# Optimization experiments

Measured on AMD Instinct MI355X. Metric: run time of the kernel, lower is better.

## Reference

```python
import jax, jax.numpy as jnp
import numpy as np

N_GT = 20000          # num_genotypes
N_T = 50              # num timepoints
N_POS = 2000          # num_positions
ALPHA = 4             # len_alphabet
TIME_STEP = 5         # spacing between consecutive timepoints (generations)
ZERO_THR = 1e-6       # hparams['zero threshold']
DILUTION = 0.3        # hparams['dilution threshold']


def setup_inputs() -> dict:
    key = jax.random.key(0)
    k1, k2, k3 = jax.random.split(key, 3)
    fitness = jnp.ones((N_GT,), jnp.float32) * -1.0 + jax.random.normal(k1, (N_GT,), jnp.float32) * 0.01
    fq_mat = jax.random.normal(k2, (N_T, N_GT), jnp.float32)
    genotypes_tensor = jax.random.bernoulli(k3, 0.5, (N_GT, N_POS * ALPHA)).astype(jnp.float32)
    return {"fitness": fitness, "fq_mat": fq_mat, "genotypes_tensor": genotypes_tensor}


def _safe_log(x, m):
    # log(x) where mask m is true, 0 elsewhere (grad-safe)
    return jnp.where(m, jnp.log(jnp.where(m, x, 1.0)), 0.0)


def reference(fitness, fq_mat, genotypes_tensor):
    fqm = jax.nn.softmax(fq_mat, axis=1)                       # (n_t, n_gt)

    # Marginals: (n_t, n_pos*alpha)
    pred_marginals = (fqm @ genotypes_tensor) / N_POS + 1e-10
    log_pred_marginals = jnp.log(pred_marginals)

    # --- Fitness loss: replicator dynamics between consecutive timepoints ---
    p0s = fqm[:-1]                                             # (n_t-1, n_gt)
    p1s = fqm[1:]                                              # (n_t-1, n_gt)
    mask = p0s >= ZERO_THR                                     # dynamic masking -> weights
    fmask = mask.astype(fqm.dtype)
    p0m = p0s * fmask
    p1m = p1s * fmask
    weight = p1m.sum(axis=1)                                   # (n_t-1,)
    np1 = p1m / weight[:, None]                                # normalized target dist

    present_fitness = jnp.exp(fitness)[None, :] * fmask        # (n_t-1, n_gt)

    # time_step replicator sub-steps (uniform spacing -> fixed unrolled loop)
    input_ps = p0m
    for _ in range(TIME_STEP):
        mean_pop_fitness = jnp.sum(input_ps * present_fitness, axis=1, keepdims=True)
        input_ps = input_ps * (present_fitness / mean_pop_fitness)

    pos = np1 > 0
    kl = jnp.sum(jnp.where(pos, np1 * (_safe_log(np1, pos) - _safe_log(input_ps, pos)), 0.0), axis=1)
    loss_t = weight * kl
    # skip timepoints with weight < dilution threshold
    fitness_loss = jnp.sum(jnp.where(weight >= DILUTION, loss_t, 0.0)) / (N_T - 1)
    fitness_loss = fitness_loss.reshape(1)

    # --- Sparsity (negative skew) loss ---
    m = fqm.mean(axis=1, keepdims=True)
    unnorm_skew = ((fqm - m) ** 3).mean(axis=1)                # (n_t,)
    fq_sparsity_loss = (-unnorm_skew.sum() / N_T).reshape(1)

    return log_pred_marginals, fitness_loss, fq_sparsity_loss
```

## Files before the change

kernel.cpp:

```cpp
#include <hip/hip_runtime.h>
#include <cfloat>
#include <cstdint>

#define N_GT 20000
#define N_T 50
#define NPA 8000
#define N_POS 2000
#define KSTEPS 625
#define KTILE 32
#define PBLK 256
#define FB 512
#define NE 40
#define SCH 2500

typedef __attribute__((ext_vector_type(8))) short short8;
typedef __attribute__((ext_vector_type(4))) float f32x4;

__device__ __forceinline__ float wave_sum(float v) {
#pragma unroll
    for (int o = 32; o > 0; o >>= 1) v += __shfl_down(v, o, 64);
    return v;
}
__device__ float block_sum(float v, float* red) {
    int lane = threadIdx.x & 63, wid = threadIdx.x >> 6, nw = blockDim.x >> 6;
    v = wave_sum(v);
    __syncthreads();
    if (lane == 0) red[wid] = v;
    __syncthreads();
    if (wid == 0) {
        float x = (lane < nw) ? red[lane] : 0.f;
        x = wave_sum(x);
        if (lane == 0) red[0] = x;
    }
    __syncthreads();
    return red[0];
}

__global__ __launch_bounds__(256) void softmax_sum_kernel(
    const float* __restrict__ fq, float* __restrict__ rowsum) {
    __shared__ float red[8];
    int row = blockIdx.x >> 3, c = blockIdx.x & 7;
    const float* p = fq + (size_t)row * N_GT + c * SCH;
    float s = 0.f;
    for (int i = threadIdx.x; i < SCH; i += 256) s += __expf(p[i]);
    s = block_sum(s, red);
    if (threadIdx.x == 0) rowsum[blockIdx.x] = s;
}

__global__ __launch_bounds__(256) void softmax_write_kernel(
    const float* __restrict__ fq, const float* __restrict__ rowsum,
    float* __restrict__ fqm, unsigned short* __restrict__ fqmb,
    float* __restrict__ out) {
    __shared__ float red[8];
    int row = blockIdx.x >> 3, c = blockIdx.x & 7;
    float S = 0.f;
#pragma unroll
    for (int j = 0; j < 8; ++j) S += rowsum[row * 8 + j];
    float inv = 1.f / S;

    const float* p = fq + (size_t)row * N_GT + c * SCH;
    float* ym = fqm + (size_t)row * N_GT + c * SCH;
    unsigned short* yb = fqmb + (size_t)row * N_GT + c * SCH;
    const float mean = 1.f / (float)N_GT;
    float skew = 0.f;
    for (int i = threadIdx.x; i < SCH; i += 256) {
        float y = __expf(p[i]) * inv;
        ym[i] = y;
        unsigned ub = __float_as_uint(y);
        yb[i] = (unsigned short)((ub + 0x7FFFu + ((ub >> 16) & 1u)) >> 16);
        float d = y - mean;
        skew += d * d * d;
    }
    skew = block_sum(skew, red);
    if (threadIdx.x == 0)
        atomicAdd(out + 400001, skew * (-1.f / ((float)N_GT * (float)N_T)));
}

__global__ __launch_bounds__(FB) void fitness_kernel(
    const float* __restrict__ fqm, const float* __restrict__ fitness,
    float* __restrict__ out) {
    __shared__ float red[8];
    int t = blockIdx.x;
    const float* p0 = fqm + (size_t)t * N_GT;
    const float* p1 = p0 + N_GT;

    float p0m[NE], p1m[NE], l5f[NE];
    float wsum = 0.f, s5 = 0.f;
#pragma unroll
    for (int j = 0; j < NE; ++j) {
        int g = threadIdx.x + j * FB;
        bool in = g < N_GT;
        float a = in ? p0[g] : 0.f;
        float b = in ? p1[g] : 0.f;
        bool m = in && (a >= 1e-6f);
        p0m[j] = m ? a : 0.f;
        p1m[j] = m ? b : 0.f;
        l5f[j] = in ? 5.f * fitness[g] : 0.f;
        wsum += p1m[j];
        s5 += p0m[j] * __expf(l5f[j]);
    }
    float weight = block_sum(wsum, red);
    float S5 = block_sum(s5, red);
    float lS5 = __logf(S5);
    float invw = 1.f / weight;

    float kls = 0.f;
#pragma unroll
    for (int j = 0; j < NE; ++j) {
        if (p1m[j] > 0.f) {
            float np1 = p1m[j] * invw;
            float lips = __logf(p0m[j]) + l5f[j] - lS5;
            kls += np1 * (__logf(np1) - lips);
        }
    }
    float kl = block_sum(kls, red);
    if (threadIdx.x == 0 && weight >= 0.3f)
        atomicAdd(out + 400000, weight * kl * (1.f / (float)(N_T - 1)));
}

__global__ __launch_bounds__(256, 2) void gemm_mfma_kernel(
    const float* __restrict__ B, const unsigned short* __restrict__ Abf,
    float* __restrict__ partial, int ch) {
    __shared__ __align__(16) float lds[2][KTILE][PBLK];
    const int tid = threadIdx.x;
    const int l = tid & 63, w = tid >> 6;
    const int ln = l & 15, kq = l >> 4;
    const int kq8 = kq * 8;
    const int woff = w * 64;
    const int pblk = blockIdx.x * PBLK;
    const int s = blockIdx.y;

    const int ks0 = s * ch;
    int ks1 = ks0 + ch; if (ks1 > KSTEPS) ks1 = KSTEPS;
    const int nk = ks1 - ks0;
    if (nk <= 0) return;

    int scol = pblk + l * 4;
    if (scol > NPA - 4) scol = NPA - 4;

    const unsigned short* abase = Abf + (size_t)ln * N_GT;

    f32x4 acc[4][4];
#pragma unroll
    for (int mt = 0; mt < 4; ++mt)
#pragma unroll
        for (int nt = 0; nt < 4; ++nt)
            acc[mt][nt] = (f32x4){0.f, 0.f, 0.f, 0.f};

    short8 a0[4], a1[4];

#define STAGE(BUF, KS) do {                                                    \
    const float* gsrc_ = B + (size_t)(KS) * (KTILE * NPA) + scol;              \
    _Pragma("unroll") for (int it_ = 0; it_ < 8; ++it_) {                      \
        int row_ = w * 8 + it_;                                                \
        __builtin_amdgcn_global_load_lds(                                      \
            (const __attribute__((address_space(1))) void*)(gsrc_ + (size_t)row_ * NPA), \
            (__attribute__((address_space(3))) void*)&lds[BUF][row_][0],       \
            16, 0, 0);                                                         \
    }                                                                          \
} while (0)

#define LOADA(AV, KS) do {                                                     \
    const int k0_ = (KS) * 32 + kq8;                                           \
    _Pragma("unroll") for (int mt_ = 0; mt_ < 4; ++mt_)                        \
        AV[mt_] = *(const short8*)(abase + (size_t)(mt_ * 16) * N_GT + k0_);   \
} while (0)

#define COMPUTE(BUF, AV) do {                                                  \
    f32x4 f_[8];                                                               \
    _Pragma("unroll") for (int j_ = 0; j_ < 8; ++j_)                           \
        f_[j_] = *(const f32x4*)&lds[BUF][kq8 + j_][woff + ln * 4];            \
    _Pragma("unroll") for (int nt_ = 0; nt_ < 4; ++nt_) {                      \
        short8 bb_;                                                            \
        _Pragma("unroll") for (int j_ = 0; j_ < 8; ++j_)                       \
            bb_[j_] = (short)(__float_as_uint(f_[j_][nt_]) >> 16);             \
        _Pragma("unroll") for (int mt_ = 0; mt_ < 4; ++mt_)                    \
            acc[mt_][nt_] = __builtin_amdgcn_mfma_f32_16x16x32_bf16(           \
                AV[mt_], bb_, acc[mt_][nt_], 0, 0, 0);                         \
    }                                                                          \
} while (0)

    STAGE(0, ks0);
    LOADA(a0, ks0);
    int i = 0;
    for (; i + 1 < nk; i += 2) {
        __syncthreads();
        STAGE(1, ks0 + i + 1);
        LOADA(a1, ks0 + i + 1);
        COMPUTE(0, a0);
        __syncthreads();
        if (i + 2 < nk) { STAGE(0, ks0 + i + 2); LOADA(a0, ks0 + i + 2); }
        COMPUTE(1, a1);
    }
    if (i < nk) {
        __syncthreads();
        COMPUTE(0, a0);
    }

#undef STAGE
#undef LOADA
#undef COMPUTE

    const int rbase = kq * 4;
    const int pst = pblk + woff + ln * 4;
    float* ps = partial + (size_t)s * (N_T * NPA);
    if (pst < NPA) {
#pragma unroll
        for (int mt = 0; mt < 4; ++mt) {
#pragma unroll
            for (int r = 0; r < 4; ++r) {
                int t = mt * 16 + rbase + r;
                if (t < N_T) {
                    float4 v = {acc[mt][0][r], acc[mt][1][r],
                                acc[mt][2][r], acc[mt][3][r]};
                    *reinterpret_cast<float4*>(ps + (size_t)t * NPA + pst) = v;
                }
            }
        }
    }
}

__global__ __launch_bounds__(256) void reduce_log_kernel(
    const float4* __restrict__ partial, float4* __restrict__ out, int ns) {
    int i = blockIdx.x * 256 + threadIdx.x;
    if (i >= (N_T * NPA) / 4) return;
    float4 s = {0.f, 0.f, 0.f, 0.f};
    for (int k = 0; k < ns; ++k) {
        float4 v = partial[(size_t)k * ((N_T * NPA) / 4) + i];
        s.x += v.x; s.y += v.y; s.z += v.z; s.w += v.w;
    }
    const float r = 1.f / (float)N_POS;
    float4 o;
    o.x = __logf(s.x * r + 1e-10f);
    o.y = __logf(s.y * r + 1e-10f);
    o.z = __logf(s.z * r + 1e-10f);
    o.w = __logf(s.w * r + 1e-10f);
    out[i] = o;
}

extern "C" void kernel_launch(void* const* d_in, const int* in_sizes, int n_in,
                              void* d_out, int out_size, void* d_ws, size_t ws_size,
                              hipStream_t stream) {
    const float* fitness = (const float*)d_in[0];
    const float* fq_mat  = (const float*)d_in[1];
    const float* geno    = (const float*)d_in[2];
    float* out = (float*)d_out;

    char* ws = (char*)d_ws;
    float* fqm           = (float*)ws;
    unsigned short* fqmb = (unsigned short*)(ws + 4000000);
    float* rowsum        = (float*)(ws + 6560000);
    float* partial       = (float*)(ws + 6561600);

    int ns = 16;
    while (ns > 1 && (size_t)6561600 + (size_t)ns * 1600000 > ws_size) ns >>= 1;
    int ch = (KSTEPS + ns - 1) / ns;

    hipMemsetAsync((char*)d_out + (size_t)400000 * sizeof(float), 0, 2 * sizeof(float), stream);
    hipMemsetAsync((char*)fqmb + (size_t)N_T * N_GT * sizeof(unsigned short), 0,
                   (size_t)14 * N_GT * sizeof(unsigned short), stream);

    hipLaunchKernelGGL(softmax_sum_kernel, dim3(N_T * 8), dim3(256), 0, stream,
                       fq_mat, rowsum);
    hipLaunchKernelGGL(softmax_write_kernel, dim3(N_T * 8), dim3(256), 0, stream,
                       fq_mat, rowsum, fqm, fqmb, out);
    hipLaunchKernelGGL(fitness_kernel, dim3(N_T - 1), dim3(FB), 0, stream,
                       fqm, fitness, out);
    hipLaunchKernelGGL(gemm_mfma_kernel, dim3(NPA / PBLK + 1, ns), dim3(256), 0, stream,
                       geno, fqmb, partial, ch);
    hipLaunchKernelGGL(reduce_log_kernel, dim3(((N_T * NPA) / 4 + 255) / 256), dim3(256), 0, stream,
                       (const float4*)partial, (float4*)out, ns);
}
```

Before: 164.5 us.

## Fuse fitness stats into softmax, split KL pass, triple-buffer GEMM with 8 K-splits

```diff
diff --git a/kernel.cpp b/kernel.cpp
--- a/kernel.cpp
+++ b/kernel.cpp
@@ -9,8 +9,7 @@
 #define KSTEPS 625
 #define KTILE 32
 #define PBLK 256
-#define FB 512
-#define NE 40
+#define NS 8
 #define SCH 2500
 
 typedef __attribute__((ext_vector_type(8))) short short8;
@@ -49,79 +48,96 @@
 
 __global__ __launch_bounds__(256) void softmax_write_kernel(
     const float* __restrict__ fq, const float* __restrict__ rowsum,
-    float* __restrict__ fqm, unsigned short* __restrict__ fqmb,
-    float* __restrict__ out) {
+    const float* __restrict__ fitv, unsigned short* __restrict__ fqmb,
+    float* __restrict__ out, float* __restrict__ pairW,
+    float* __restrict__ pairS5) {
     __shared__ float red[8];
     int row = blockIdx.x >> 3, c = blockIdx.x & 7;
     float S = 0.f;
 #pragma unroll
     for (int j = 0; j < 8; ++j) S += rowsum[row * 8 + j];
     float inv = 1.f / S;
-
-    const float* p = fq + (size_t)row * N_GT + c * SCH;
-    float* ym = fqm + (size_t)row * N_GT + c * SCH;
+    bool hasPair = row < N_T - 1;
+    float invn = 0.f;
+    if (hasPair) {
+        float Sn = 0.f;
+#pragma unroll
+        for (int j = 0; j < 8; ++j) Sn += rowsum[(row + 1) * 8 + j];
+        invn = 1.f / Sn;
+    }
+
+    const float* p  = fq + (size_t)row * N_GT + c * SCH;
+    const float* p1 = p + N_GT;
+    const float* fv = fitv + c * SCH;
     unsigned short* yb = fqmb + (size_t)row * N_GT + c * SCH;
     const float mean = 1.f / (float)N_GT;
-    float skew = 0.f;
+    float skew = 0.f, wsum = 0.f, s5 = 0.f;
     for (int i = threadIdx.x; i < SCH; i += 256) {
         float y = __expf(p[i]) * inv;
-        ym[i] = y;
         unsigned ub = __float_as_uint(y);
         yb[i] = (unsigned short)((ub + 0x7FFFu + ((ub >> 16) & 1u)) >> 16);
         float d = y - mean;
         skew += d * d * d;
+        if (hasPair) {
+            bool m = y >= 1e-6f;
+            float y1 = __expf(p1[i]) * invn;
+            float e5 = __expf(5.f * fv[i]);
+            wsum += m ? y1 : 0.f;
+            s5   += m ? y * e5 : 0.f;
+        }
     }
     skew = block_sum(skew, red);
     if (threadIdx.x == 0)
         atomicAdd(out + 400001, skew * (-1.f / ((float)N_GT * (float)N_T)));
-}
-
-__global__ __launch_bounds__(FB) void fitness_kernel(
-    const float* __restrict__ fqm, const float* __restrict__ fitness,
-    float* __restrict__ out) {
+    if (hasPair) {
+        wsum = block_sum(wsum, red);
+        s5 = block_sum(s5, red);
+        if (threadIdx.x == 0) {
+            atomicAdd(&pairW[row], wsum);
+            atomicAdd(&pairS5[row], s5);
+        }
+    }
+}
+
+__global__ __launch_bounds__(256) void fit2_kernel(
+    const float* __restrict__ fq, const float* __restrict__ rowsum,
+    const float* __restrict__ fitv, const float* __restrict__ pairW,
+    const float* __restrict__ pairS5, float* __restrict__ out) {
     __shared__ float red[8];
-    int t = blockIdx.x;
-    const float* p0 = fqm + (size_t)t * N_GT;
-    const float* p1 = p0 + N_GT;
-
-    float p0m[NE], p1m[NE], l5f[NE];
-    float wsum = 0.f, s5 = 0.f;
-#pragma unroll
-    for (int j = 0; j < NE; ++j) {
-        int g = threadIdx.x + j * FB;
-        bool in = g < N_GT;
-        float a = in ? p0[g] : 0.f;
-        float b = in ? p1[g] : 0.f;
-        bool m = in && (a >= 1e-6f);
-        p0m[j] = m ? a : 0.f;
-        p1m[j] = m ? b : 0.f;
-        l5f[j] = in ? 5.f * fitness[g] : 0.f;
-        wsum += p1m[j];
-        s5 += p0m[j] * __expf(l5f[j]);
-    }
-    float weight = block_sum(wsum, red);
-    float S5 = block_sum(s5, red);
-    float lS5 = __logf(S5);
+    int t = blockIdx.x >> 3, c = blockIdx.x & 7;
+    float weight = pairW[t];
+    if (weight < 0.3f) return;
+    float S = 0.f, Sn = 0.f;
+#pragma unroll
+    for (int j = 0; j < 8; ++j) {
+        S  += rowsum[t * 8 + j];
+        Sn += rowsum[(t + 1) * 8 + j];
+    }
+    float inv = 1.f / S, invn = 1.f / Sn;
     float invw = 1.f / weight;
-
+    float lS5 = __logf(pairS5[t]);
+
+    const float* q0 = fq + (size_t)t * N_GT + c * SCH;
+    const float* q1 = q0 + N_GT;
+    const float* fv = fitv + c * SCH;
     float kls = 0.f;
-#pragma unroll
-    for (int j = 0; j < NE; ++j) {
-        if (p1m[j] > 0.f) {
-            float np1 = p1m[j] * invw;
-            float lips = __logf(p0m[j]) + l5f[j] - lS5;
-            kls += np1 * (__logf(np1) - lips);
-        }
-    }
-    float kl = block_sum(kls, red);
-    if (threadIdx.x == 0 && weight >= 0.3f)
-        atomicAdd(out + 400000, weight * kl * (1.f / (float)(N_T - 1)));
-}
-
-__global__ __launch_bounds__(256, 2) void gemm_mfma_kernel(
+    for (int i = threadIdx.x; i < SCH; i += 256) {
+        float y = __expf(q0[i]) * inv;
+        if (y >= 1e-6f) {
+            float y1 = __expf(q1[i]) * invn;
+            float np1 = y1 * invw;
+            kls += np1 * (__logf(np1) - (__logf(y) + 5.f * fv[i] - lS5));
+        }
+    }
+    kls = block_sum(kls, red);
+    if (threadIdx.x == 0)
+        atomicAdd(out + 400000, weight * kls * (1.f / (float)(N_T - 1)));
+}
+
+__global__ __launch_bounds__(256, 1) void gemm_mfma_kernel(
     const float* __restrict__ B, const unsigned short* __restrict__ Abf,
     float* __restrict__ partial, int ch) {
-    __shared__ __align__(16) float lds[2][KTILE][PBLK];
+    __shared__ __align__(16) float lds[3][KTILE][PBLK];
     const int tid = threadIdx.x;
     const int l = tid & 63, w = tid >> 6;
     const int ln = l & 15, kq = l >> 4;
@@ -147,7 +163,7 @@
         for (int nt = 0; nt < 4; ++nt)
             acc[mt][nt] = (f32x4){0.f, 0.f, 0.f, 0.f};
 
-    short8 a0[4], a1[4];
+    short8 avA[4], avB[4];
 
 #define STAGE(BUF, KS) do {                                                    \
     const float* gsrc_ = B + (size_t)(KS) * (KTILE * NPA) + scol;              \
@@ -181,20 +197,25 @@
 } while (0)
 
     STAGE(0, ks0);
-    LOADA(a0, ks0);
-    int i = 0;
-    for (; i + 1 < nk; i += 2) {
-        __syncthreads();
-        STAGE(1, ks0 + i + 1);
-        LOADA(a1, ks0 + i + 1);
-        COMPUTE(0, a0);
-        __syncthreads();
-        if (i + 2 < nk) { STAGE(0, ks0 + i + 2); LOADA(a0, ks0 + i + 2); }
-        COMPUTE(1, a1);
-    }
-    if (i < nk) {
-        __syncthreads();
-        COMPUTE(0, a0);
+    if (nk > 1) STAGE(1, ks0 + 1);
+    LOADA(avA, ks0);
+
+    int cur = 0;
+#pragma unroll 1
+    for (int i = 0; i < nk; ++i) {
+        if (i < nk - 1) asm volatile("s_waitcnt vmcnt(8)" ::: "memory");
+        else            asm volatile("s_waitcnt vmcnt(0)" ::: "memory");
+        __builtin_amdgcn_s_barrier();
+        asm volatile("" ::: "memory");
+        if (i + 1 < nk) {
+            if (i & 1) LOADA(avA, ks0 + i + 1); else LOADA(avB, ks0 + i + 1);
+        }
+        if (i + 2 < nk) {
+            int nb = cur + 2; if (nb >= 3) nb -= 3;
+            STAGE(nb, ks0 + i + 2);
+        }
+        if (i & 1) COMPUTE(cur, avB); else COMPUTE(cur, avA);
+        ++cur; if (cur == 3) cur = 0;
     }
 
 #undef STAGE
@@ -247,27 +268,27 @@
     float* out = (float*)d_out;
 
     char* ws = (char*)d_ws;
-    float* fqm           = (float*)ws;
-    unsigned short* fqmb = (unsigned short*)(ws + 4000000);
-    float* rowsum        = (float*)(ws + 6560000);
-    float* partial       = (float*)(ws + 6561600);
-
-    int ns = 16;
-    while (ns > 1 && (size_t)6561600 + (size_t)ns * 1600000 > ws_size) ns >>= 1;
-    int ch = (KSTEPS + ns - 1) / ns;
+    unsigned short* fqmb = (unsigned short*)ws;
+    float* rowsum        = (float*)(ws + 2560000);
+    float* pairW         = (float*)(ws + 2561600);
+    float* pairS5        = (float*)(ws + 2561856);
+    float* partial       = (float*)(ws + 2564096);
+
+    const int ch = (KSTEPS + NS - 1) / NS;
 
     hipMemsetAsync((char*)d_out + (size_t)400000 * sizeof(float), 0, 2 * sizeof(float), stream);
+    hipMemsetAsync(ws + 2561600, 0, 512, stream);
     hipMemsetAsync((char*)fqmb + (size_t)N_T * N_GT * sizeof(unsigned short), 0,
                    (size_t)14 * N_GT * sizeof(unsigned short), stream);
 
     hipLaunchKernelGGL(softmax_sum_kernel, dim3(N_T * 8), dim3(256), 0, stream,
                        fq_mat, rowsum);
     hipLaunchKernelGGL(softmax_write_kernel, dim3(N_T * 8), dim3(256), 0, stream,
-                       fq_mat, rowsum, fqm, fqmb, out);
-    hipLaunchKernelGGL(fitness_kernel, dim3(N_T - 1), dim3(FB), 0, stream,
-                       fqm, fitness, out);
-    hipLaunchKernelGGL(gemm_mfma_kernel, dim3(NPA / PBLK + 1, ns), dim3(256), 0, stream,
+                       fq_mat, rowsum, fitness, fqmb, out, pairW, pairS5);
+    hipLaunchKernelGGL(fit2_kernel, dim3((N_T - 1) * 8), dim3(256), 0, stream,
+                       fq_mat, rowsum, fitness, pairW, pairS5, out);
+    hipLaunchKernelGGL(gemm_mfma_kernel, dim3((NPA + PBLK - 1) / PBLK, NS), dim3(256), 0, stream,
                        geno, fqmb, partial, ch);
     hipLaunchKernelGGL(reduce_log_kernel, dim3(((N_T * NPA) / 4 + 255) / 256), dim3(256), 0, stream,
-                       (const float4*)partial, (float4*)out, ns);
-}
+                       (const float4*)partial, (float4*)out, NS);
+}
```

After: 202.4 us. 23.0% more time.
